# Kernel optimization log

Hardware: AMD Instinct MI355X
Metric: run time of the kernel (lower is better)

The kernel has to match this reference:

```python
import jax, jax.numpy as jnp
from jax import lax
import numpy as np

B, SQ, SK, H, NH, KS = 2, 2048, 2048, 1024, 16, 3
D = H // NH  # depth per head = 64


def setup_inputs() -> dict:
    key = jax.random.key(0)
    ks = jax.random.split(key, 10)
    s = 0.02
    return {
        "query_input": jax.random.normal(ks[0], (B, SQ, H), jnp.float32),
        "source_input": jax.random.normal(ks[1], (B, SK, H), jnp.float32),
        "mask": jnp.zeros((B, 1, 1, SK), jnp.float32),
        "Wq": jax.random.normal(ks[2], (KS, H, H), jnp.float32) * s,
        "bq": jnp.zeros((H,), jnp.float32),
        "Wk": jax.random.normal(ks[3], (KS, H, H), jnp.float32) * s,
        "bk": jnp.zeros((H,), jnp.float32),
        "Wv": jax.random.normal(ks[4], (KS, H, H), jnp.float32) * s,
        "bv": jnp.zeros((H,), jnp.float32),
        "Wo": jax.random.normal(ks[5], (H, H), jnp.float32) * s,
        "bo": jnp.zeros((H,), jnp.float32),
    }


def _conv1d_same(x, W, b):
    # x: [B, S, H], W: [KS, H_in, H_out] -> 'same' padded 1D conv
    y = lax.conv_general_dilated(x, W, window_strides=(1,), padding="SAME",
                                 dimension_numbers=("NWC", "WIO", "NWC"))
    return y + b


def _split_heads(x):
    # [B, S, H] -> [B, NH, S, D]
    b, s, _ = x.shape
    return x.reshape(b, s, NH, D).transpose(0, 2, 1, 3)


def reference(query_input, source_input, mask, Wq, bq, Wk, bk, Wv, bv, Wo, bo):
    q = _split_heads(_conv1d_same(query_input, Wq, bq)) * (D ** -0.5)
    k = _split_heads(_conv1d_same(source_input, Wk, bk))
    v = _split_heads(_conv1d_same(source_input, Wv, bv))
    logits = jnp.einsum("bhqd,bhkd->bhqk", q, k) + mask * (-1e9)
    weights = jax.nn.softmax(logits, axis=-1)  # dropout omitted (eval mode)
    attn = jnp.einsum("bhqk,bhkd->bhqd", weights, v)
    attn = attn.transpose(0, 2, 1, 3).reshape(q.shape[0], -1, H)
    return attn @ Wo + bo
```

## Files before the change

### kernel.cpp

```cpp
#include <hip/hip_runtime.h>
#include <stdint.h>

#define B_   2
#define S_   2048
#define H_   1024
#define NH_  16
#define D_   64
#define KC_  3072

typedef __attribute__((ext_vector_type(8))) short  short8;
typedef __attribute__((ext_vector_type(4))) float  floatx4;

typedef __attribute__((address_space(1))) const void gas_void;
typedef __attribute__((address_space(3))) void       las_void;

__device__ __forceinline__ void gld16(const void* g, void* l) {
    __builtin_amdgcn_global_load_lds((gas_void*)g, (las_void*)l, 16, 0, 0);
}

__device__ __forceinline__ unsigned short f2bf(float f) {
    union { float f; unsigned u; } v; v.f = f;
    unsigned r = v.u + 0x7fffu + ((v.u >> 16) & 1u);
    return (unsigned short)(r >> 16);
}

__global__ __launch_bounds__(256) void k_pad_convert(const float* __restrict__ src,
                                                     unsigned short* __restrict__ dst) {
    int gid = blockIdx.x * 256 + threadIdx.x;
    int vid = gid * 4;
    if (vid >= B_ * 2050 * 1024) return;
    int row = vid >> 10;
    int b   = (row >= 2050) ? 1 : 0;
    int r   = row - b * 2050;
    int h   = vid & 1023;
    unsigned short o0 = 0, o1 = 0, o2 = 0, o3 = 0;
    if (r != 0 && r != 2049) {
        const float4 f = *(const float4*)(src + ((b * 2048 + r - 1) << 10) + h);
        o0 = f2bf(f.x); o1 = f2bf(f.y); o2 = f2bf(f.z); o3 = f2bf(f.w);
    }
    ushort4 o; o.x = o0; o.y = o1; o.z = o2; o.w = o3;
    *(ushort4*)(dst + vid) = o;
}

__global__ void k_transpose_bf16(const float* __restrict__ src,
                                 unsigned short* __restrict__ dst, int R, int C) {
    __shared__ float t[32][33];
    int c0 = blockIdx.x * 32, r0 = blockIdx.y * 32;
    int tx = threadIdx.x, ty = threadIdx.y;
#pragma unroll
    for (int k = 0; k < 4; ++k)
        t[ty + k * 8][tx] = src[(long)(r0 + ty + k * 8) * C + c0 + tx];
    __syncthreads();
#pragma unroll
    for (int k = 0; k < 4; ++k)
        dst[(long)(c0 + ty + k * 8) * R + r0 + tx] = f2bf(t[tx][ty + k * 8]);
}

__global__ __launch_bounds__(256) void k_conv_gemm(
    const unsigned short* __restrict__ xq, const unsigned short* __restrict__ xs,
    const unsigned short* __restrict__ Wqt, const unsigned short* __restrict__ Wkt,
    const unsigned short* __restrict__ Wvt,
    const float* __restrict__ bq, const float* __restrict__ bk, const float* __restrict__ bv,
    unsigned short* __restrict__ Qo, unsigned short* __restrict__ Ko,
    unsigned short* __restrict__ Vo) {
    int z = blockIdx.z;
    const unsigned short* X = (z == 0) ? xq : xs;
    const unsigned short* W = (z == 0) ? Wqt : (z == 1 ? Wkt : Wvt);
    const float* bias = (z == 0) ? bq : (z == 1 ? bk : bv);

    __shared__ unsigned short Al[132 * 64];
    __shared__ unsigned short Bl[3 * 128 * 64];

    int n0 = blockIdx.x * 128, m0 = blockIdx.y * 128;
    int b = m0 >> 11;
    int tid = threadIdx.x, lane = tid & 63, w = tid >> 6;
    int quad = lane >> 4, l15 = lane & 15;
    int wm = w >> 1, wn = w & 1;

    floatx4 acc[4][4];
#pragma unroll
    for (int i = 0; i < 4; ++i)
#pragma unroll
        for (int j = 0; j < 4; ++j) acc[i][j] = (floatx4){0.f, 0.f, 0.f, 0.f};

    const unsigned short* Xbase = X + (m0 + 2 * b) * 1024;

    int eaA[4], oaA[4];
#pragma unroll
    for (int it = 0; it < 4; ++it) {
        int e  = (it * 256 + tid) * 8;
        int r  = e >> 6;
        int cp = (e >> 3) & 7;
        int c  = cp ^ (r & 7);
        eaA[it] = e;
        oaA[it] = r * 1024 + c * 8;
    }
    int eaX = 0, oaX = 0;
    if (tid < 16) {
        int e  = (1024 + tid) * 8;
        int r  = 128 + (tid >> 3);
        int cp = tid & 7;
        int c  = cp ^ (r & 7);
        eaX = e;
        oaX = r * 1024 + c * 8;
    }
    int eaB[12], oaB[12];
#pragma unroll
    for (int it = 0; it < 12; ++it) {
        int e  = (it * 256 + tid) * 8;
        int t  = e >> 13;
        int er = e & 8191;
        int rl = er >> 6;
        int cp = (er >> 3) & 7;
        int c  = cp ^ (rl & 7);
        eaB[it] = e;
        oaB[it] = (n0 + rl) * KC_ + t * 1024 + c * 8;
    }

    for (int kt = 0; kt < 16; ++kt) {
        int k0 = kt * 64;
#pragma unroll
        for (int it = 0; it < 4; ++it)
            gld16(Xbase + oaA[it] + k0, (char*)Al + eaA[it] * 2);
        if (tid < 16)
            gld16(Xbase + oaX + k0, (char*)Al + eaX * 2);
#pragma unroll
        for (int it = 0; it < 12; ++it)
            gld16(W + oaB[it] + k0, (char*)Bl + eaB[it] * 2);
        __syncthreads();

#pragma unroll
        for (int t = 0; t < 3; ++t) {
#pragma unroll
            for (int kk = 0; kk < 2; ++kk) {
                short8 af[4], bf[4];
#pragma unroll
                for (int i = 0; i < 4; ++i) {
                    int r  = wm * 64 + i * 16 + l15 + t;
                    int cp = (kk * 4 + quad) ^ (r & 7);
                    af[i]  = *(const short8*)(Al + r * 64 + cp * 8);
                }
#pragma unroll
                for (int j = 0; j < 4; ++j) {
                    int n  = wn * 64 + j * 16 + l15;
                    int cp = (kk * 4 + quad) ^ (n & 7);
                    bf[j]  = *(const short8*)(Bl + t * 8192 + n * 64 + cp * 8);
                }
#pragma unroll
                for (int i = 0; i < 4; ++i)
#pragma unroll
                    for (int j = 0; j < 4; ++j)
                        acc[i][j] = __builtin_amdgcn_mfma_f32_16x16x32_bf16(af[i], bf[j], acc[i][j], 0, 0, 0);
            }
        }
        __syncthreads();
    }

#pragma unroll
    for (int j = 0; j < 4; ++j) {
        int n = n0 + wn * 64 + j * 16 + l15;
        float bb = bias[n];
        int nh = n >> 6, d = n & 63;
#pragma unroll
        for (int i = 0; i < 4; ++i) {
            int srow = (m0 & 2047) + wm * 64 + i * 16 + quad * 4;
#pragma unroll
            for (int r = 0; r < 4; ++r) {
                float v = acc[i][j][r] + bb;
                int s = srow + r;
                if (z == 0)
                    Qo[((b * NH_ + nh) * 2048 + s) * 64 + d] = f2bf(v * 0.125f);
                else if (z == 1)
                    Ko[((b * NH_ + nh) * 2048 + s) * 64 + d] = f2bf(v);
                else
                    Vo[((b * NH_ + nh) * 64 + d) * 2048 + s] = f2bf(v);
            }
        }
    }
}

__global__ __launch_bounds__(256) void k_flash(
    const unsigned short* __restrict__ Q, const unsigned short* __restrict__ K,
    const unsigned short* __restrict__ Vt, const float* __restrict__ mask,
    unsigned short* __restrict__ Ao) {
    __shared__ unsigned short Ul[128 * 136];
    __shared__ unsigned short Vl[64 * 128];

    int tid = threadIdx.x, w = tid >> 6, lane = tid & 63;
    int quad = lane >> 4, l15 = lane & 15;
    int bh = blockIdx.y;
    int b = bh >> 4, nh = bh & 15;
    int q0 = blockIdx.x * 128, wq = w * 32;

    short8 qf[2][2];
#pragma unroll
    for (int i = 0; i < 2; ++i)
#pragma unroll
        for (int kk = 0; kk < 2; ++kk)
            qf[i][kk] = *(const short8*)(Q + ((bh * 2048 + q0 + wq + i * 16 + l15) << 6) + kk * 32 + quad * 8);

    floatx4 oacc[2][4];
    float rsum[2][4];
#pragma unroll
    for (int i = 0; i < 2; ++i) {
#pragma unroll
        for (int j = 0; j < 4; ++j) oacc[i][j] = (floatx4){0.f, 0.f, 0.f, 0.f};
#pragma unroll
        for (int r = 0; r < 4; ++r) rsum[i][r] = 0.f;
    }
    const float* maskb = mask + b * S_;

    for (int kt = 0; kt < 16; ++kt) {
        int k0 = kt * 128;
#pragma unroll
        for (int it = 0; it < 4; ++it) {
            int e  = (it * 256 + tid) * 8;
            int kl = e >> 6;
            int c  = ((e >> 3) & 7) ^ (kl & 7);
            gld16(K + (bh * 2048 + k0 + kl) * 64 + c * 8, (char*)Ul + e * 2);
            int dl = e >> 7;
            int cp = (e >> 3) & 15;
            int c2 = (cp & 8) | ((cp ^ dl) & 7);
            gld16(Vt + (bh * 64 + dl) * 2048 + k0 + c2 * 8, (char*)Vl + e * 2);
        }
        __syncthreads();

        floatx4 sacc[2][8];
#pragma unroll
        for (int i = 0; i < 2; ++i)
#pragma unroll
            for (int j = 0; j < 8; ++j) sacc[i][j] = (floatx4){0.f, 0.f, 0.f, 0.f};
#pragma unroll
        for (int j = 0; j < 8; ++j) {
            int kl = j * 16 + l15;
            int cp0 = (0 * 4 + quad) ^ (kl & 7);
            short8 bf0 = *(const short8*)(Ul + kl * 64 + cp0 * 8);
            int cp1 = (1 * 4 + quad) ^ (kl & 7);
            short8 bf1 = *(const short8*)(Ul + kl * 64 + cp1 * 8);
#pragma unroll
            for (int i = 0; i < 2; ++i) {
                sacc[i][j] = __builtin_amdgcn_mfma_f32_16x16x32_bf16(qf[i][0], bf0, sacc[i][j], 0, 0, 0);
                sacc[i][j] = __builtin_amdgcn_mfma_f32_16x16x32_bf16(qf[i][1], bf1, sacc[i][j], 0, 0, 0);
            }
        }
        __syncthreads();

#pragma unroll
        for (int j = 0; j < 8; ++j) {
            float mv = maskb[k0 + j * 16 + l15] * (-1e9f);
#pragma unroll
            for (int i = 0; i < 2; ++i) {
                int row = wq + i * 16 + quad * 4;
#pragma unroll
                for (int r = 0; r < 4; ++r) {
                    float p = __expf(sacc[i][j][r] + mv);
                    rsum[i][r] += p;
                    Ul[(row + r) * 136 + j * 16 + l15] = f2bf(p);
                }
            }
        }

#pragma unroll
        for (int kk = 0; kk < 4; ++kk) {
            short8 af[2], bv4[4];
#pragma unroll
            for (int i = 0; i < 2; ++i)
                af[i] = *(const short8*)(Ul + (wq + i * 16 + l15) * 136 + kk * 32 + quad * 8);
#pragma unroll
            for (int j2 = 0; j2 < 4; ++j2) {
                int dl = j2 * 16 + l15;
                int c  = kk * 4 + quad;
                int cp = (c & 8) | ((c ^ dl) & 7);
                bv4[j2] = *(const short8*)(Vl + dl * 128 + cp * 8);
            }
#pragma unroll
            for (int i = 0; i < 2; ++i)
#pragma unroll
                for (int j2 = 0; j2 < 4; ++j2)
                    oacc[i][j2] = __builtin_amdgcn_mfma_f32_16x16x32_bf16(af[i], bv4[j2], oacc[i][j2], 0, 0, 0);
        }
        __syncthreads();
    }

#pragma unroll
    for (int i = 0; i < 2; ++i)
#pragma unroll
        for (int r = 0; r < 4; ++r) {
            float v = rsum[i][r];
            v += __shfl_xor(v, 1); v += __shfl_xor(v, 2);
            v += __shfl_xor(v, 4); v += __shfl_xor(v, 8);
            rsum[i][r] = 1.0f / v;
        }

#pragma unroll
    for (int i = 0; i < 2; ++i)
#pragma unroll
        for (int j2 = 0; j2 < 4; ++j2)
#pragma unroll
            for (int r = 0; r < 4; ++r) {
                int qrow = q0 + wq + i * 16 + quad * 4 + r;
                int hcol = nh * 64 + j2 * 16 + l15;
                Ao[(b * 2048 + qrow) * 1024 + hcol] = f2bf(oacc[i][j2][r] * rsum[i][r]);
            }
}

__global__ __launch_bounds__(256) void k_proj_gemm(
    const unsigned short* __restrict__ A, const unsigned short* __restrict__ Wt,
    const float* __restrict__ bo, float* __restrict__ out) {
    __shared__ unsigned short Al[2][128 * 64];
    __shared__ unsigned short Bl[2][128 * 64];

    int n0 = blockIdx.x * 128, m0 = blockIdx.y * 128;
    int tid = threadIdx.x, lane = tid & 63, w = tid >> 6;
    int quad = lane >> 4, l15 = lane & 15;
    int wm = w >> 1, wn = w & 1;

    floatx4 acc[4][4];
#pragma unroll
    for (int i = 0; i < 4; ++i)
#pragma unroll
        for (int j = 0; j < 4; ++j) acc[i][j] = (floatx4){0.f, 0.f, 0.f, 0.f};

    int eoff[4], aoff[4], boff[4];
#pragma unroll
    for (int it = 0; it < 4; ++it) {
        int e  = (it * 256 + tid) * 8;
        int rl = e >> 6;
        int c  = ((e >> 3) & 7) ^ (rl & 7);
        eoff[it] = e;
        aoff[it] = (m0 + rl) * 1024 + c * 8;
        boff[it] = (n0 + rl) * 1024 + c * 8;
    }

    auto stage = [&](int buf, int k0) {
#pragma unroll
        for (int it = 0; it < 4; ++it) {
            gld16(A + aoff[it] + k0, (char*)Al[buf] + eoff[it] * 2);
            gld16(Wt + boff[it] + k0, (char*)Bl[buf] + eoff[it] * 2);
        }
    };
    auto compute = [&](int buf) {
#pragma unroll
        for (int kk = 0; kk < 2; ++kk) {
            short8 af[4], bf[4];
#pragma unroll
            for (int i = 0; i < 4; ++i) {
                int m  = wm * 64 + i * 16 + l15;
                int cp = (kk * 4 + quad) ^ (m & 7);
                af[i]  = *(const short8*)(Al[buf] + m * 64 + cp * 8);
            }
#pragma unroll
            for (int j = 0; j < 4; ++j) {
                int n  = wn * 64 + j * 16 + l15;
                int cp = (kk * 4 + quad) ^ (n & 7);
                bf[j]  = *(const short8*)(Bl[buf] + n * 64 + cp * 8);
            }
#pragma unroll
            for (int i = 0; i < 4; ++i)
#pragma unroll
                for (int j = 0; j < 4; ++j)
                    acc[i][j] = __builtin_amdgcn_mfma_f32_16x16x32_bf16(af[i], bf[j], acc[i][j], 0, 0, 0);
        }
    };

    stage(0, 0);
    __syncthreads();
    for (int kt = 0; kt < 16; kt += 2) {
        if (kt + 1 < 16) stage(1, (kt + 1) * 64);
        compute(0);
        __syncthreads();
        if (kt + 2 < 16) stage(0, (kt + 2) * 64);
        compute(1);
        __syncthreads();
    }

#pragma unroll
    for (int j = 0; j < 4; ++j) {
        int n = n0 + wn * 64 + j * 16 + l15;
        float bb = bo[n];
#pragma unroll
        for (int i = 0; i < 4; ++i) {
            int m = m0 + wm * 64 + i * 16 + quad * 4;
#pragma unroll
            for (int r = 0; r < 4; ++r)
                out[(m + r) * 1024 + n] = acc[i][j][r] + bb;
        }
    }
}

extern "C" void kernel_launch(void* const* d_in, const int* in_sizes, int n_in,
                              void* d_out, int out_size, void* d_ws, size_t ws_size,
                              hipStream_t stream) {
    (void)in_sizes; (void)n_in; (void)out_size; (void)ws_size;
    const float* q_in = (const float*)d_in[0];
    const float* s_in = (const float*)d_in[1];
    const float* mask = (const float*)d_in[2];
    const float* Wq   = (const float*)d_in[3];
    const float* bq   = (const float*)d_in[4];
    const float* Wk   = (const float*)d_in[5];
    const float* bk   = (const float*)d_in[6];
    const float* Wv   = (const float*)d_in[7];
    const float* bv   = (const float*)d_in[8];
    const float* Wo   = (const float*)d_in[9];
    const float* bo   = (const float*)d_in[10];
    float* out = (float*)d_out;

    char* ws = (char*)d_ws;
    size_t off = 0;
    auto alloc = [&](size_t bytes) {
        char* p = ws + off;
        off += (bytes + 255) & ~(size_t)255;
        return p;
    };
    unsigned short* xqp = (unsigned short*)alloc((size_t)B_ * 2050 * 1024 * 2);
    unsigned short* xsp = (unsigned short*)alloc((size_t)B_ * 2050 * 1024 * 2);
    unsigned short* Wqt = (unsigned short*)alloc((size_t)KC_ * H_ * 2);
    unsigned short* Wkt = (unsigned short*)alloc((size_t)KC_ * H_ * 2);
    unsigned short* Wvt = (unsigned short*)alloc((size_t)KC_ * H_ * 2);
    unsigned short* Wot = (unsigned short*)alloc((size_t)H_ * H_ * 2);
    unsigned short* Qb  = (unsigned short*)alloc((size_t)B_ * NH_ * S_ * D_ * 2);
    unsigned short* Kb  = (unsigned short*)alloc((size_t)B_ * NH_ * S_ * D_ * 2);
    unsigned short* Vtb = (unsigned short*)alloc((size_t)B_ * NH_ * S_ * D_ * 2);
    unsigned short* Ab  = (unsigned short*)alloc((size_t)B_ * S_ * H_ * 2);

    k_pad_convert<<<4100, 256, 0, stream>>>(q_in, xqp);
    k_pad_convert<<<4100, 256, 0, stream>>>(s_in, xsp);
    k_transpose_bf16<<<dim3(32, 96), dim3(32, 8), 0, stream>>>(Wq, Wqt, KC_, H_);
    k_transpose_bf16<<<dim3(32, 96), dim3(32, 8), 0, stream>>>(Wk, Wkt, KC_, H_);
    k_transpose_bf16<<<dim3(32, 96), dim3(32, 8), 0, stream>>>(Wv, Wvt, KC_, H_);
    k_transpose_bf16<<<dim3(32, 32), dim3(32, 8), 0, stream>>>(Wo, Wot, H_, H_);
    k_conv_gemm<<<dim3(8, 32, 3), 256, 0, stream>>>(xqp, xsp, Wqt, Wkt, Wvt,
                                                    bq, bk, bv, Qb, Kb, Vtb);
    k_flash<<<dim3(16, 32), 256, 0, stream>>>(Qb, Kb, Vtb, mask, Ab);
    k_proj_gemm<<<dim3(8, 32), 256, 0, stream>>>(Ab, Wot, bo, out);
}
```

Measured before the change: 314.3 us.

## Restructure conv GEMM into 256x256 double-buffered pipelined tiles with implicit im2col

The Q/K/V conv GEMM moves from 128x128 tiles with 256 threads to 256x256 tiles with 512 threads and double-buffered LDS. Global-to-LDS loads for later k-steps are interleaved with MFMA phases, using explicit barriers, waitcnt and setprio. The three conv taps are folded into one K=3072 loop that reads contiguous overlapping rows of the padded input, replacing the separate per-tap handling. The intent is more data reuse per tile and hiding load latency behind compute. The trade-off is a grid of only 192 blocks, which may underfill the GPU's CUs.

```diff
diff --git a/kernel.cpp b/kernel.cpp
--- a/kernel.cpp
+++ b/kernel.cpp
@@ -56,7 +56,7 @@
         dst[(long)(c0 + ty + k * 8) * R + r0 + tx] = f2bf(t[tx][ty + k * 8]);
 }
 
-__global__ __launch_bounds__(256) void k_conv_gemm(
+__global__ __launch_bounds__(512, 2) void k_conv_gemm(
     const unsigned short* __restrict__ xq, const unsigned short* __restrict__ xs,
     const unsigned short* __restrict__ Wqt, const unsigned short* __restrict__ Wkt,
     const unsigned short* __restrict__ Wvt,
@@ -68,92 +68,121 @@
     const unsigned short* W = (z == 0) ? Wqt : (z == 1 ? Wkt : Wvt);
     const float* bias = (z == 0) ? bq : (z == 1 ? bk : bv);
 
-    __shared__ unsigned short Al[132 * 64];
-    __shared__ unsigned short Bl[3 * 128 * 64];
-
-    int n0 = blockIdx.x * 128, m0 = blockIdx.y * 128;
+    __shared__ unsigned short Al[2][2][256 * 32];
+    __shared__ unsigned short Bl[2][2][256 * 32];
+
+    int n0 = blockIdx.x * 256, m0 = blockIdx.y * 256;
     int b = m0 >> 11;
     int tid = threadIdx.x, lane = tid & 63, w = tid >> 6;
     int quad = lane >> 4, l15 = lane & 15;
-    int wm = w >> 1, wn = w & 1;
-
-    floatx4 acc[4][4];
-#pragma unroll
-    for (int i = 0; i < 4; ++i)
+    int wm = w >> 2, wn = w & 3;
+
+    floatx4 acc[8][4];
+#pragma unroll
+    for (int i = 0; i < 8; ++i)
 #pragma unroll
         for (int j = 0; j < 4; ++j) acc[i][j] = (floatx4){0.f, 0.f, 0.f, 0.f};
 
-    const unsigned short* Xbase = X + (m0 + 2 * b) * 1024;
-
-    int eaA[4], oaA[4];
-#pragma unroll
-    for (int it = 0; it < 4; ++it) {
-        int e  = (it * 256 + tid) * 8;
-        int r  = e >> 6;
-        int cp = (e >> 3) & 7;
-        int c  = cp ^ (r & 7);
-        eaA[it] = e;
-        oaA[it] = r * 1024 + c * 8;
-    }
-    int eaX = 0, oaX = 0;
-    if (tid < 16) {
-        int e  = (1024 + tid) * 8;
-        int r  = 128 + (tid >> 3);
-        int cp = tid & 7;
-        int c  = cp ^ (r & 7);
-        eaX = e;
-        oaX = r * 1024 + c * 8;
-    }
-    int eaB[12], oaB[12];
-#pragma unroll
-    for (int it = 0; it < 12; ++it) {
-        int e  = (it * 256 + tid) * 8;
-        int t  = e >> 13;
-        int er = e & 8191;
-        int rl = er >> 6;
-        int cp = (er >> 3) & 7;
-        int c  = cp ^ (rl & 7);
-        eaB[it] = e;
-        oaB[it] = (n0 + rl) * KC_ + t * 1024 + c * 8;
-    }
-
-    for (int kt = 0; kt < 16; ++kt) {
-        int k0 = kt * 64;
-#pragma unroll
-        for (int it = 0; it < 4; ++it)
-            gld16(Xbase + oaA[it] + k0, (char*)Al + eaA[it] * 2);
-        if (tid < 16)
-            gld16(Xbase + oaX + k0, (char*)Al + eaX * 2);
-#pragma unroll
-        for (int it = 0; it < 12; ++it)
-            gld16(W + oaB[it] + k0, (char*)Bl + eaB[it] * 2);
-        __syncthreads();
-
-#pragma unroll
-        for (int t = 0; t < 3; ++t) {
-#pragma unroll
-            for (int kk = 0; kk < 2; ++kk) {
-                short8 af[4], bf[4];
-#pragma unroll
-                for (int i = 0; i < 4; ++i) {
-                    int r  = wm * 64 + i * 16 + l15 + t;
-                    int cp = (kk * 4 + quad) ^ (r & 7);
-                    af[i]  = *(const short8*)(Al + r * 64 + cp * 8);
-                }
-#pragma unroll
-                for (int j = 0; j < 4; ++j) {
-                    int n  = wn * 64 + j * 16 + l15;
-                    int cp = (kk * 4 + quad) ^ (n & 7);
-                    bf[j]  = *(const short8*)(Bl + t * 8192 + n * 64 + cp * 8);
-                }
-#pragma unroll
-                for (int i = 0; i < 4; ++i)
-#pragma unroll
-                    for (int j = 0; j < 4; ++j)
-                        acc[i][j] = __builtin_amdgcn_mfma_f32_16x16x32_bf16(af[i], bf[j], acc[i][j], 0, 0, 0);
-            }
-        }
-        __syncthreads();
+    const unsigned short* Xb = X + (m0 + 2 * b) * 1024;
+
+    int e0 = tid, e1 = 512 + tid;
+    int ra0 = e0 >> 2, ca0 = (e0 & 3) ^ ((e0 >> 3) & 3);
+    int ra1 = e1 >> 2, ca1 = (e1 & 3) ^ ((e1 >> 3) & 3);
+    const unsigned short* aS0 = Xb + ra0 * 1024 + ca0 * 8;
+    const unsigned short* aS1 = Xb + ra1 * 1024 + ca1 * 8;
+    const unsigned short* bS0 = W + (long)(n0 + ra0) * KC_ + ca0 * 8;
+    const unsigned short* bS1 = W + (long)(n0 + ra1) * KC_ + ca1 * 8;
+    int ld0 = tid * 16, ld1 = (512 + tid) * 16;
+
+    auto stA = [&](int kt, int kh) {
+        int o = kt * 64 + kh * 32;
+        char* d = (char*)Al + (((kt & 1) * 2 + kh) << 14);
+        gld16(aS0 + o, d + ld0);
+        gld16(aS1 + o, d + ld1);
+    };
+    auto stB = [&](int kt, int kh) {
+        int o = kt * 64 + kh * 32;
+        char* d = (char*)Bl + (((kt & 1) * 2 + kh) << 14);
+        gld16(bS0 + o, d + ld0);
+        gld16(bS1 + o, d + ld1);
+    };
+
+    int xsw = (quad ^ ((l15 >> 1) & 3)) * 16;
+    const char* ldsAb = (const char*)Al + wm * 8192 + l15 * 64 + xsw;
+    const char* ldsBb = (const char*)Bl + wn * 4096 + l15 * 64 + xsw;
+
+#define LDA(BUF, KK, I) (*(const short8*)(ldsAb + (((BUF) * 2 + (KK)) << 14) + (I) * 1024))
+#define LDB(BUF, KK, J) (*(const short8*)(ldsBb + (((BUF) * 2 + (KK)) << 14) + (J) * 1024))
+#define PH_MFMA(IH) \
+    __builtin_amdgcn_s_setprio(1); \
+    _Pragma("unroll") \
+    for (int ii = 0; ii < 4; ++ii) \
+        _Pragma("unroll") \
+        for (int j = 0; j < 4; ++j) \
+            acc[(IH) * 4 + ii][j] = __builtin_amdgcn_mfma_f32_16x16x32_bf16( \
+                af[ii], bfr[j], acc[(IH) * 4 + ii][j], 0, 0, 0); \
+    __builtin_amdgcn_s_setprio(0);
+#define BARX() __builtin_amdgcn_s_barrier()
+#define LGKM0() asm volatile("s_waitcnt lgkmcnt(0)" ::: "memory")
+#define VM10()  asm volatile("s_waitcnt vmcnt(10)" ::: "memory")
+
+    stB(0, 0); stA(0, 0); stB(0, 1); stA(0, 1); stB(1, 0); stA(1, 0); stB(1, 1);
+    VM10();
+    BARX();
+
+#define TILE(KT, BUF) do { \
+    short8 af[4], bfr[4]; \
+     \
+    bfr[0] = LDB(BUF, 0, 0); bfr[1] = LDB(BUF, 0, 1); bfr[2] = LDB(BUF, 0, 2); bfr[3] = LDB(BUF, 0, 3); \
+    af[0] = LDA(BUF, 0, 0); af[1] = LDA(BUF, 0, 1); af[2] = LDA(BUF, 0, 2); af[3] = LDA(BUF, 0, 3); \
+    stA((KT) + 1, 1); \
+    BARX(); LGKM0(); \
+    PH_MFMA(0) \
+    BARX(); \
+     \
+    af[0] = LDA(BUF, 0, 4); af[1] = LDA(BUF, 0, 5); af[2] = LDA(BUF, 0, 6); af[3] = LDA(BUF, 0, 7); \
+    stB((KT) + 2, 0); \
+    BARX(); LGKM0(); \
+    PH_MFMA(1) \
+    VM10();  \
+    BARX(); \
+     \
+    bfr[0] = LDB(BUF, 1, 0); bfr[1] = LDB(BUF, 1, 1); bfr[2] = LDB(BUF, 1, 2); bfr[3] = LDB(BUF, 1, 3); \
+    af[0] = LDA(BUF, 1, 0); af[1] = LDA(BUF, 1, 1); af[2] = LDA(BUF, 1, 2); af[3] = LDA(BUF, 1, 3); \
+    stA((KT) + 2, 0); \
+    BARX(); LGKM0(); \
+    PH_MFMA(0) \
+    BARX(); \
+     \
+    af[0] = LDA(BUF, 1, 4); af[1] = LDA(BUF, 1, 5); af[2] = LDA(BUF, 1, 6); af[3] = LDA(BUF, 1, 7); \
+    stB((KT) + 2, 1); \
+    BARX(); LGKM0(); \
+    PH_MFMA(1) \
+    VM10();  \
+    BARX(); \
+} while (0)
+
+    for (int kt = 0; kt < 46; kt += 2) {
+        TILE(kt, 0);
+        TILE(kt + 1, 1);
+    }
+
+    stA(47, 1);
+    asm volatile("s_waitcnt vmcnt(0)" ::: "memory");
+    BARX();
+    {
+        short8 af[4], bfr[4];
+#define TAILK(BUF, KK) \
+        bfr[0] = LDB(BUF, KK, 0); bfr[1] = LDB(BUF, KK, 1); bfr[2] = LDB(BUF, KK, 2); bfr[3] = LDB(BUF, KK, 3); \
+        af[0] = LDA(BUF, KK, 0); af[1] = LDA(BUF, KK, 1); af[2] = LDA(BUF, KK, 2); af[3] = LDA(BUF, KK, 3); \
+        PH_MFMA(0) \
+        af[0] = LDA(BUF, KK, 4); af[1] = LDA(BUF, KK, 5); af[2] = LDA(BUF, KK, 6); af[3] = LDA(BUF, KK, 7); \
+        PH_MFMA(1)
+        TAILK(0, 0)
+        TAILK(0, 1)
+        TAILK(1, 0)
+        TAILK(1, 1)
+#undef TAILK
     }
 
 #pragma unroll
@@ -162,8 +191,8 @@
         float bb = bias[n];
         int nh = n >> 6, d = n & 63;
 #pragma unroll
-        for (int i = 0; i < 4; ++i) {
-            int srow = (m0 & 2047) + wm * 64 + i * 16 + quad * 4;
+        for (int i = 0; i < 8; ++i) {
+            int srow = (m0 & 2047) + wm * 128 + i * 16 + quad * 4;
 #pragma unroll
             for (int r = 0; r < 4; ++r) {
                 float v = acc[i][j][r] + bb;
@@ -177,6 +206,13 @@
             }
         }
     }
+#undef TILE
+#undef LDA
+#undef LDB
+#undef PH_MFMA
+#undef BARX
+#undef LGKM0
+#undef VM10
 }
 
 __global__ __launch_bounds__(256) void k_flash(
@@ -429,7 +465,7 @@
     k_transpose_bf16<<<dim3(32, 96), dim3(32, 8), 0, stream>>>(Wk, Wkt, KC_, H_);
     k_transpose_bf16<<<dim3(32, 96), dim3(32, 8), 0, stream>>>(Wv, Wvt, KC_, H_);
     k_transpose_bf16<<<dim3(32, 32), dim3(32, 8), 0, stream>>>(Wo, Wot, H_, H_);
-    k_conv_gemm<<<dim3(8, 32, 3), 256, 0, stream>>>(xqp, xsp, Wqt, Wkt, Wvt,
+    k_conv_gemm<<<dim3(4, 16, 3), 512, 0, stream>>>(xqp, xsp, Wqt, Wkt, Wvt,
                                                     bq, bk, bv, Qb, Kb, Vtb);
     k_flash<<<dim3(16, 32), 256, 0, stream>>>(Qb, Kb, Vtb, mask, Ab);
     k_proj_gemm<<<dim3(8, 32), 256, 0, stream>>>(Ab, Wot, bo, out);
```

Result: slower. 336.3 us (+7.0%).

## Flatten conv GEMM taps into a single 3072-deep K loop with small LDS tiles

Applied to the files above, without the earlier changes.

The 3-tap conv GEMM no longer stages a 132-row input tile reused by all three taps alongside a 3-tap weight tile. It now runs 48 K-steps, each loading one 128x64 input tile and one 128x64 weight tile. The tap shift is handled implicitly: the K offset runs past the 1024-wide row into the following padded input rows. This cuts LDS use from about 64KB to 32KB per block, allowing more blocks per CU. In exchange it drops the input-tile reuse across taps, roughly tripling activation loads, and triples the number of barriers per block.

```diff
diff --git a/kernel.cpp b/kernel.cpp
--- a/kernel.cpp
+++ b/kernel.cpp
@@ -68,8 +68,8 @@
     const unsigned short* W = (z == 0) ? Wqt : (z == 1 ? Wkt : Wvt);
     const float* bias = (z == 0) ? bq : (z == 1 ? bk : bv);
 
-    __shared__ unsigned short Al[132 * 64];
-    __shared__ unsigned short Bl[3 * 128 * 64];
+    __shared__ unsigned short Al[128 * 64];
+    __shared__ unsigned short Bl[128 * 64];
 
     int n0 = blockIdx.x * 128, m0 = blockIdx.y * 128;
     int b = m0 >> 11;
@@ -83,75 +83,48 @@
 #pragma unroll
         for (int j = 0; j < 4; ++j) acc[i][j] = (floatx4){0.f, 0.f, 0.f, 0.f};
 
-    const unsigned short* Xbase = X + (m0 + 2 * b) * 1024;
-
-    int eaA[4], oaA[4];
+    const unsigned short* Xb = X + (m0 + 2 * b) * 1024;
+
+    int eoff[4], aoff[4], boff[4];
 #pragma unroll
     for (int it = 0; it < 4; ++it) {
         int e  = (it * 256 + tid) * 8;
-        int r  = e >> 6;
-        int cp = (e >> 3) & 7;
-        int c  = cp ^ (r & 7);
-        eaA[it] = e;
-        oaA[it] = r * 1024 + c * 8;
-    }
-    int eaX = 0, oaX = 0;
-    if (tid < 16) {
-        int e  = (1024 + tid) * 8;
-        int r  = 128 + (tid >> 3);
-        int cp = tid & 7;
-        int c  = cp ^ (r & 7);
-        eaX = e;
-        oaX = r * 1024 + c * 8;
-    }
-    int eaB[12], oaB[12];
-#pragma unroll
-    for (int it = 0; it < 12; ++it) {
-        int e  = (it * 256 + tid) * 8;
-        int t  = e >> 13;
-        int er = e & 8191;
-        int rl = er >> 6;
-        int cp = (er >> 3) & 7;
-        int c  = cp ^ (rl & 7);
-        eaB[it] = e;
-        oaB[it] = (n0 + rl) * KC_ + t * 1024 + c * 8;
-    }
-
-    for (int kt = 0; kt < 16; ++kt) {
+        int rl = e >> 6;
+        int c  = ((e >> 3) & 7) ^ (rl & 7);
+        eoff[it] = e;
+        aoff[it] = rl * 1024 + c * 8;
+        boff[it] = (n0 + rl) * KC_ + c * 8;
+    }
+
+    for (int kt = 0; kt < 48; ++kt) {
         int k0 = kt * 64;
 #pragma unroll
-        for (int it = 0; it < 4; ++it)
-            gld16(Xbase + oaA[it] + k0, (char*)Al + eaA[it] * 2);
-        if (tid < 16)
-            gld16(Xbase + oaX + k0, (char*)Al + eaX * 2);
-#pragma unroll
-        for (int it = 0; it < 12; ++it)
-            gld16(W + oaB[it] + k0, (char*)Bl + eaB[it] * 2);
-        __syncthreads();
-
-#pragma unroll
-        for (int t = 0; t < 3; ++t) {
-#pragma unroll
-            for (int kk = 0; kk < 2; ++kk) {
-                short8 af[4], bf[4];
-#pragma unroll
-                for (int i = 0; i < 4; ++i) {
-                    int r  = wm * 64 + i * 16 + l15 + t;
-                    int cp = (kk * 4 + quad) ^ (r & 7);
-                    af[i]  = *(const short8*)(Al + r * 64 + cp * 8);
-                }
-#pragma unroll
-                for (int j = 0; j < 4; ++j) {
-                    int n  = wn * 64 + j * 16 + l15;
-                    int cp = (kk * 4 + quad) ^ (n & 7);
-                    bf[j]  = *(const short8*)(Bl + t * 8192 + n * 64 + cp * 8);
-                }
-#pragma unroll
-                for (int i = 0; i < 4; ++i)
-#pragma unroll
-                    for (int j = 0; j < 4; ++j)
-                        acc[i][j] = __builtin_amdgcn_mfma_f32_16x16x32_bf16(af[i], bf[j], acc[i][j], 0, 0, 0);
-            }
+        for (int it = 0; it < 4; ++it) {
+            gld16(Xb + aoff[it] + k0, (char*)Al + eoff[it] * 2);
+            gld16(W + boff[it] + k0, (char*)Bl + eoff[it] * 2);
+        }
+        __syncthreads();
+
+#pragma unroll
+        for (int kk = 0; kk < 2; ++kk) {
+            short8 af[4], bf[4];
+#pragma unroll
+            for (int i = 0; i < 4; ++i) {
+                int m  = wm * 64 + i * 16 + l15;
+                int cp = (kk * 4 + quad) ^ (m & 7);
+                af[i]  = *(const short8*)(Al + m * 64 + cp * 8);
+            }
+#pragma unroll
+            for (int j = 0; j < 4; ++j) {
+                int n  = wn * 64 + j * 16 + l15;
+                int cp = (kk * 4 + quad) ^ (n & 7);
+                bf[j]  = *(const short8*)(Bl + n * 64 + cp * 8);
+            }
+#pragma unroll
+            for (int i = 0; i < 4; ++i)
+#pragma unroll
+                for (int j = 0; j < 4; ++j)
+                    acc[i][j] = __builtin_amdgcn_mfma_f32_16x16x32_bf16(af[i], bf[j], acc[i][j], 0, 0, 0);
         }
         __syncthreads();
     }
```

Measured after the change: 359.5 us. +14.4%, slower.

## Read K/V directly from global in flash kernel, drop shared staging and barriers

Applied to the files above, without the earlier changes.

The flash attention kernel stops staging K and V tiles in shared memory and instead loads MFMA operands straight from global memory, relying on L2/cache reuse. Blocks shrink to 128 threads (64 query rows), each wave gets a private P buffer so all __syncthreads are removed, and blocks are remapped so the 8 blocks of the same head land on different XCD slots for better cache sharing. This trades global load traffic and latency for fewer barriers and higher occupancy, and risks redundant K/V reads across waves.

```diff
diff --git a/kernel.cpp b/kernel.cpp
--- a/kernel.cpp
+++ b/kernel.cpp
@@ -179,18 +179,24 @@
     }
 }
 
-__global__ __launch_bounds__(256) void k_flash(
+__global__ __launch_bounds__(128) void k_flash(
     const unsigned short* __restrict__ Q, const unsigned short* __restrict__ K,
     const unsigned short* __restrict__ Vt, const float* __restrict__ mask,
     unsigned short* __restrict__ Ao) {
-    __shared__ unsigned short Ul[128 * 136];
-    __shared__ unsigned short Vl[64 * 128];
+    __shared__ unsigned short Pl[2][32 * 136];
 
     int tid = threadIdx.x, w = tid >> 6, lane = tid & 63;
     int quad = lane >> 4, l15 = lane & 15;
-    int bh = blockIdx.y;
+
+    int p  = blockIdx.x + 32 * blockIdx.y;
+    int l  = (p & 7) * 128 + (p >> 3);
+    int bh = l >> 5, qx = l & 31;
     int b = bh >> 4, nh = bh & 15;
-    int q0 = blockIdx.x * 128, wq = w * 32;
+    int q0 = qx * 64, wq = w * 32;
+
+    const unsigned short* Kb = K + bh * 2048 * 64;
+    const unsigned short* Vb = Vt + bh * 64 * 2048;
+    unsigned short* Pw = &Pl[w][0];
 
     short8 qf[2][2];
 #pragma unroll
@@ -212,18 +218,6 @@
 
     for (int kt = 0; kt < 16; ++kt) {
         int k0 = kt * 128;
-#pragma unroll
-        for (int it = 0; it < 4; ++it) {
-            int e  = (it * 256 + tid) * 8;
-            int kl = e >> 6;
-            int c  = ((e >> 3) & 7) ^ (kl & 7);
-            gld16(K + (bh * 2048 + k0 + kl) * 64 + c * 8, (char*)Ul + e * 2);
-            int dl = e >> 7;
-            int cp = (e >> 3) & 15;
-            int c2 = (cp & 8) | ((cp ^ dl) & 7);
-            gld16(Vt + (bh * 64 + dl) * 2048 + k0 + c2 * 8, (char*)Vl + e * 2);
-        }
-        __syncthreads();
 
         floatx4 sacc[2][8];
 #pragma unroll
@@ -233,29 +227,27 @@
 #pragma unroll
         for (int j = 0; j < 8; ++j) {
             int kl = j * 16 + l15;
-            int cp0 = (0 * 4 + quad) ^ (kl & 7);
-            short8 bf0 = *(const short8*)(Ul + kl * 64 + cp0 * 8);
-            int cp1 = (1 * 4 + quad) ^ (kl & 7);
-            short8 bf1 = *(const short8*)(Ul + kl * 64 + cp1 * 8);
+            const unsigned short* kr = Kb + (k0 + kl) * 64 + quad * 8;
+            short8 bf0 = *(const short8*)(kr);
+            short8 bf1 = *(const short8*)(kr + 32);
 #pragma unroll
             for (int i = 0; i < 2; ++i) {
                 sacc[i][j] = __builtin_amdgcn_mfma_f32_16x16x32_bf16(qf[i][0], bf0, sacc[i][j], 0, 0, 0);
                 sacc[i][j] = __builtin_amdgcn_mfma_f32_16x16x32_bf16(qf[i][1], bf1, sacc[i][j], 0, 0, 0);
             }
         }
-        __syncthreads();
 
 #pragma unroll
         for (int j = 0; j < 8; ++j) {
             float mv = maskb[k0 + j * 16 + l15] * (-1e9f);
 #pragma unroll
             for (int i = 0; i < 2; ++i) {
-                int row = wq + i * 16 + quad * 4;
+                int row = i * 16 + quad * 4;
 #pragma unroll
                 for (int r = 0; r < 4; ++r) {
-                    float p = __expf(sacc[i][j][r] + mv);
-                    rsum[i][r] += p;
-                    Ul[(row + r) * 136 + j * 16 + l15] = f2bf(p);
+                    float pv = __expf(sacc[i][j][r] + mv);
+                    rsum[i][r] += pv;
+                    Pw[(row + r) * 136 + j * 16 + l15] = f2bf(pv);
                 }
             }
         }
@@ -265,13 +257,11 @@
             short8 af[2], bv4[4];
 #pragma unroll
             for (int i = 0; i < 2; ++i)
-                af[i] = *(const short8*)(Ul + (wq + i * 16 + l15) * 136 + kk * 32 + quad * 8);
+                af[i] = *(const short8*)(Pw + (i * 16 + l15) * 136 + kk * 32 + quad * 8);
 #pragma unroll
             for (int j2 = 0; j2 < 4; ++j2) {
                 int dl = j2 * 16 + l15;
-                int c  = kk * 4 + quad;
-                int cp = (c & 8) | ((c ^ dl) & 7);
-                bv4[j2] = *(const short8*)(Vl + dl * 128 + cp * 8);
+                bv4[j2] = *(const short8*)(Vb + dl * 2048 + k0 + (kk * 4 + quad) * 8);
             }
 #pragma unroll
             for (int i = 0; i < 2; ++i)
@@ -279,7 +269,6 @@
                 for (int j2 = 0; j2 < 4; ++j2)
                     oacc[i][j2] = __builtin_amdgcn_mfma_f32_16x16x32_bf16(af[i], bv4[j2], oacc[i][j2], 0, 0, 0);
         }
-        __syncthreads();
     }
 
 #pragma unroll
@@ -431,6 +420,6 @@
     k_transpose_bf16<<<dim3(32, 32), dim3(32, 8), 0, stream>>>(Wo, Wot, H_, H_);
     k_conv_gemm<<<dim3(8, 32, 3), 256, 0, stream>>>(xqp, xsp, Wqt, Wkt, Wvt,
                                                     bq, bk, bv, Qb, Kb, Vtb);
-    k_flash<<<dim3(16, 32), 256, 0, stream>>>(Qb, Kb, Vtb, mask, Ab);
+    k_flash<<<dim3(32, 32), 128, 0, stream>>>(Qb, Kb, Vtb, mask, Ab);
     k_proj_gemm<<<dim3(8, 32), 256, 0, stream>>>(Ab, Wot, bo, out);
 }
```

After: 405.4 us. +29.0%, slower.
